# Optimization experiments

Measured on AMD Instinct MI355X. Metric: run time of the kernel, lower is better.

## Reference

```python
import jax, jax.numpy as jnp
import numpy as np

B, DZ, H, DY = 4096, 512, 2048, 10
N_STEPS = 64
SCALE = 0.02  # matches param_ulow/uhigh magnitude


def setup_inputs() -> dict:
    key = jax.random.key(0)
    ks = jax.random.split(key, 6)
    x = jax.random.normal(ks[0], (B, DZ), dtype=jnp.float32)
    A = jax.random.normal(ks[1], (DZ, DZ), dtype=jnp.float32) * SCALE
    W1 = jax.random.normal(ks[2], (H, DZ), dtype=jnp.float32) * SCALE
    b1 = jax.random.normal(ks[3], (H,), dtype=jnp.float32) * SCALE
    W2 = jax.random.normal(ks[4], (DY, H), dtype=jnp.float32) * SCALE
    b2 = jax.random.normal(ks[5], (DY,), dtype=jnp.float32) * SCALE
    return {"x": x, "A": A, "W1": W1, "b1": b1, "W2": W2, "b2": b2,
            "n_steps": N_STEPS}


def reference(x, A, W1, b1, W2, b2, n_steps):
    # Z0 = P @ x with P = I  => Z0 = x
    # dz/dt = einsum('ji,bi->bj', A, z) = z @ A.T ; explicit Euler on [0, 1]
    dt = jnp.float32(1.0 / n_steps)

    def euler_step(z, _):
        return z + dt * (z @ A.T), None

    zT, _ = jax.lax.scan(euler_step, x, None, length=n_steps)  # [B, DZ]
    # Q MLP (n_layers=3): Linear -> ReLU -> Linear
    h = jax.nn.relu(zT @ W1.T + b1)  # [B, H]
    y = h @ W2.T + b2                # [B, DY]
    return y
```

## Files before the change

### kernel.cpp

```cpp
#include <hip/hip_runtime.h>
#include <hip/hip_bf16.h>

#define B_SZ 4096
#define DZ   512
#define H_SZ 2048
#define DY   10

#define C2 0.4921875f
#define C3 0.158935546875f
#define C4 0.037872314453125f
#define C5 ((float)(7624512.0/1073741824.0))
#define C6 ((float)(74974368.0/68719476736.0))

typedef __attribute__((ext_vector_type(8))) __bf16 bf16x8;
typedef __attribute__((ext_vector_type(4))) float  f32x4;
typedef __attribute__((ext_vector_type(8))) unsigned short us8;

__device__ inline unsigned short f2bf(float f) {
    unsigned u = __float_as_uint(f);
    u += 0x7fffu + ((u >> 16) & 1u);
    return (unsigned short)(u >> 16);
}
__device__ inline float bf2f(unsigned short s) {
    return __uint_as_float(((unsigned)s) << 16);
}

__device__ __forceinline__ void gl16(const void* g, void* l) {
    __builtin_amdgcn_global_load_lds(
        (const __attribute__((address_space(1))) unsigned int*)(size_t)g,
        (__attribute__((address_space(3))) unsigned int*)(unsigned)(size_t)l,
        16, 0, 0);
}

union SqSmem {
    struct { unsigned short A[64 * 64]; unsigned short B[64 * 64]; } s;
    float epi[64 * 68];
};

__device__ __forceinline__ void stage64(const unsigned short* __restrict__ src,
                                        unsigned short* lds, int row_base,
                                        int kt, int t) {
    const int w = t >> 6, lane = t & 63;
#pragma unroll
    for (int i = 0; i < 2; ++i) {
        int o = w * 128 + i * 64 + lane;
        int row = o >> 3, cc = (o & 7) ^ (row & 7);
        gl16(&src[(size_t)(row_base + row) * 512 + kt * 64 + cc * 8],
             &lds[(size_t)(w * 128 + i * 64) * 8]);
    }
}

#define MFMA_STEP(acc)                                                        \
    {                                                                         \
        _Pragma("unroll")                                                     \
        for (int ks = 0; ks < 2; ++ks) {                                      \
            bf16x8 af[2], bfr[2];                                             \
            _Pragma("unroll")                                                 \
            for (int i = 0; i < 2; ++i) {                                     \
                int ra = wm + i * 16 + l16, ca = (ks * 4 + quad) ^ (ra & 7);  \
                af[i] = *(const bf16x8*)&sm.s.A[ra * 64 + ca * 8];            \
                int rb = wn + i * 16 + l16, cb = (ks * 4 + quad) ^ (rb & 7);  \
                bfr[i] = *(const bf16x8*)&sm.s.B[rb * 64 + cb * 8];           \
            }                                                                 \
            _Pragma("unroll")                                                 \
            for (int i = 0; i < 2; ++i)                                       \
                _Pragma("unroll")                                             \
                for (int j = 0; j < 2; ++j)                                   \
                    acc[i][j] = __builtin_amdgcn_mfma_f32_16x16x32_bf16(      \
                        af[i], bfr[j], acc[i][j], 0, 0, 0);                   \
        }                                                                     \
    }

#define ACC_TO_EPI(acc)                                                       \
    {                                                                         \
        _Pragma("unroll")                                                     \
        for (int i = 0; i < 2; ++i)                                           \
            _Pragma("unroll")                                                 \
            for (int j = 0; j < 2; ++j)                                       \
                _Pragma("unroll")                                             \
                for (int rr = 0; rr < 4; ++rr)                                \
                    sm.epi[(wm + i * 16 + quad * 4 + rr) * 68 +               \
                           wn + j * 16 + l16] = acc[i][j][rr];                \
        __syncthreads();                                                      \
    }

__device__ inline void gemm64_mfma(const unsigned short* __restrict__ Arows,
                                   const unsigned short* __restrict__ Brows,
                                   int m0, int n0, int t, SqSmem& sm) {
    const int lane = t & 63, w = t >> 6, quad = lane >> 4, l16 = lane & 15;
    const int wm = (w & 1) * 32, wn = (w >> 1) * 32;
    f32x4 acc[2][2];
#pragma unroll
    for (int i = 0; i < 2; ++i)
#pragma unroll
        for (int j = 0; j < 2; ++j) acc[i][j] = (f32x4){0.f, 0.f, 0.f, 0.f};
    for (int kt = 0; kt < 8; ++kt) {
        stage64(Arows, sm.s.A, m0, kt, t);
        stage64(Brows, sm.s.B, n0, kt, t);
        __syncthreads();
        MFMA_STEP(acc)
        __syncthreads();
    }
    ACC_TO_EPI(acc)
}

__device__ inline void gemm64_f32src(const float* __restrict__ Arows,
                                     const float* __restrict__ Bsrc,
                                     int m0, int n0, int t, SqSmem& sm) {
    const int lane = t & 63, w = t >> 6, quad = lane >> 4, l16 = lane & 15;
    const int wm = (w & 1) * 32, wn = (w >> 1) * 32;
    const int r = t >> 2, cq = t & 3;
    f32x4 acc[2][2];
#pragma unroll
    for (int i = 0; i < 2; ++i)
#pragma unroll
        for (int j = 0; j < 2; ++j) acc[i][j] = (f32x4){0.f, 0.f, 0.f, 0.f};
    for (int kt = 0; kt < 8; ++kt) {
        float va[16];
#pragma unroll
        for (int u = 0; u < 4; ++u) {
            float4 f = *(const float4*)&Arows[(size_t)(m0 + r) * 512 + kt * 64 + cq * 16 + u * 4];
            va[u * 4 + 0] = f.x; va[u * 4 + 1] = f.y;
            va[u * 4 + 2] = f.z; va[u * 4 + 3] = f.w;
        }
#pragma unroll
        for (int j2 = 0; j2 < 2; ++j2) {
            us8 h;
#pragma unroll
            for (int j = 0; j < 8; ++j) h[j] = f2bf(va[j2 * 8 + j]);
            int cc = cq * 2 + j2;
            *(us8*)&sm.s.A[r * 64 + (cc ^ (r & 7)) * 8] = h;
        }
#pragma unroll
        for (int u = 0; u < 4; ++u) {
            float4 f = *(const float4*)&Bsrc[(size_t)(kt * 64 + r) * 512 + n0 + cq * 16 + u * 4];
            float vv[4] = {f.x, f.y, f.z, f.w};
#pragma unroll
            for (int j = 0; j < 4; ++j) {
                int n = cq * 16 + u * 4 + j;
                sm.s.B[n * 64 + ((r >> 3) ^ (n & 7)) * 8 + (r & 7)] = f2bf(vv[j]);
            }
        }
        __syncthreads();
        MFMA_STEP(acc)
        __syncthreads();
    }
    ACC_TO_EPI(acc)
}

__device__ inline void epi_out_bf(unsigned short* __restrict__ dst, int m0,
                                  int n0, int t, SqSmem& sm) {
    const int r = t >> 2, cq = t & 3;
    us8 h0, h1;
#pragma unroll
    for (int j = 0; j < 8; ++j) {
        h0[j] = f2bf(sm.epi[r * 68 + cq * 16 + j]);
        h1[j] = f2bf(sm.epi[r * 68 + cq * 16 + 8 + j]);
    }
    *(us8*)&dst[(size_t)(m0 + r) * 512 + n0 + cq * 16]     = h0;
    *(us8*)&dst[(size_t)(m0 + r) * 512 + n0 + cq * 16 + 8] = h1;
}
__device__ inline void epi_out_bfT(unsigned short* __restrict__ dst, int m0,
                                   int n0, int t, SqSmem& sm) {
    const int cf = t >> 2, rq = t & 3;
    us8 o0, o1;
#pragma unroll
    for (int i = 0; i < 8; ++i) {
        o0[i] = f2bf(sm.epi[(rq * 16 + i) * 68 + cf]);
        o1[i] = f2bf(sm.epi[(rq * 16 + 8 + i) * 68 + cf]);
    }
    *(us8*)&dst[(size_t)(n0 + cf) * 512 + m0 + rq * 16]     = o0;
    *(us8*)&dst[(size_t)(n0 + cf) * 512 + m0 + rq * 16 + 8] = o1;
}

__global__ __launch_bounds__(256) void k_s1(
    const float* __restrict__ A, const float* __restrict__ x,
    const float* __restrict__ W1, const float* __restrict__ b2,
    unsigned short* __restrict__ A2_bf, unsigned short* __restrict__ A2T_bf,
    unsigned short* __restrict__ AT_bf, unsigned short* __restrict__ A_bf,
    unsigned short* __restrict__ x_bf, unsigned short* __restrict__ W1_bf,
    float* __restrict__ y) {
    __shared__ SqSmem sm;
    const int b = blockIdx.x, t = threadIdx.x;

    if (b < 64) {
        const int m0 = (b >> 3) * 64, n0 = (b & 7) * 64;
        gemm64_f32src(A, A, m0, n0, t, sm);
        epi_out_bf(A2_bf, m0, n0, t, sm);
        epi_out_bfT(A2T_bf, m0, n0, t, sm);
    } else if (b < 128) {
        const int bb = b - 64, m0 = (bb >> 3) * 64, n0 = (bb & 7) * 64;
        const int r = t >> 2, cq = t & 3;
#pragma unroll
        for (int u = 0; u < 4; ++u) {
            float4 f = *(const float4*)&A[(size_t)(m0 + r) * 512 + n0 + cq * 16 + u * 4];
            sm.epi[r * 68 + cq * 16 + u * 4 + 0] = f.x;
            sm.epi[r * 68 + cq * 16 + u * 4 + 1] = f.y;
            sm.epi[r * 68 + cq * 16 + u * 4 + 2] = f.z;
            sm.epi[r * 68 + cq * 16 + u * 4 + 3] = f.w;
        }
        __syncthreads();
        epi_out_bfT(AT_bf, m0, n0, t, sm);
    } else {
        const int gid = (b - 128) * 256 + t;
        const float4* x4 = (const float4*)x;
#pragma unroll
        for (int i = 0; i < 8; ++i) {
            int id = gid + i * 32768;
            float4 v0 = x4[(size_t)id * 2], v1 = x4[(size_t)id * 2 + 1];
            us8 o;
            o[0] = f2bf(v0.x); o[1] = f2bf(v0.y); o[2] = f2bf(v0.z); o[3] = f2bf(v0.w);
            o[4] = f2bf(v1.x); o[5] = f2bf(v1.y); o[6] = f2bf(v1.z); o[7] = f2bf(v1.w);
            *(us8*)&x_bf[(size_t)id * 8] = o;
        }
        const float4* w4 = (const float4*)W1;
#pragma unroll
        for (int i = 0; i < 4; ++i) {
            int id = gid + i * 32768;
            float4 v0 = w4[(size_t)id * 2], v1 = w4[(size_t)id * 2 + 1];
            us8 o;
            o[0] = f2bf(v0.x); o[1] = f2bf(v0.y); o[2] = f2bf(v0.z); o[3] = f2bf(v0.w);
            o[4] = f2bf(v1.x); o[5] = f2bf(v1.y); o[6] = f2bf(v1.z); o[7] = f2bf(v1.w);
            *(us8*)&W1_bf[(size_t)id * 8] = o;
        }
        {
            const float4* a4 = (const float4*)A;
            float4 v0 = a4[(size_t)gid * 2], v1 = a4[(size_t)gid * 2 + 1];
            us8 o;
            o[0] = f2bf(v0.x); o[1] = f2bf(v0.y); o[2] = f2bf(v0.z); o[3] = f2bf(v0.w);
            o[4] = f2bf(v1.x); o[5] = f2bf(v1.y); o[6] = f2bf(v1.z); o[7] = f2bf(v1.w);
            *(us8*)&A_bf[(size_t)gid * 8] = o;
        }
#pragma unroll
        for (int i = 0; i < 2; ++i) {
            int id = gid + i * 32768;
            if (id < B_SZ * DY) y[id] = b2[id % 10];
        }
    }
}

__global__ __launch_bounds__(256) void k_s2(
    const unsigned short* __restrict__ A2_bf,
    const unsigned short* __restrict__ A2T_bf,
    unsigned short* __restrict__ A4T_bf) {
    __shared__ SqSmem sm;
    const int b = blockIdx.x, t = threadIdx.x;
    const int m0 = (b >> 3) * 64, n0 = (b & 7) * 64;
    gemm64_mfma(A2_bf, A2T_bf, m0, n0, t, sm);
    epi_out_bfT(A4T_bf, m0, n0, t, sm);
}

__global__ __launch_bounds__(256) void k_s3(
    const unsigned short* __restrict__ A_bf,
    const unsigned short* __restrict__ A2_bf,
    const unsigned short* __restrict__ A2T_bf,
    const unsigned short* __restrict__ A4T_bf,
    const unsigned short* __restrict__ AT_bf,
    unsigned short* __restrict__ QpT_bf) {
    __shared__ SqSmem sm;
    const int b = blockIdx.x, t = threadIdx.x;
    const int m0 = (b >> 3) * 64, n0 = (b & 7) * 64;
    const int lane = t & 63, w = t >> 6, quad = lane >> 4, l16 = lane & 15;
    const int wm = (w & 1) * 32, wn = (w >> 1) * 32;
    f32x4 acc[2][2];
#pragma unroll
    for (int i = 0; i < 2; ++i)
#pragma unroll
        for (int j = 0; j < 2; ++j) acc[i][j] = (f32x4){0.f, 0.f, 0.f, 0.f};

#pragma unroll
    for (int pass = 0; pass < 2; ++pass) {
        const unsigned short* __restrict__ Bt = pass ? A4T_bf : A2T_bf;
        const float cA  = pass ? C5 : C3;
        const float cA2 = pass ? C6 : C4;
        for (int kt = 0; kt < 8; ++kt) {
            stage64(Bt, sm.s.B, n0, kt, t);
#pragma unroll
            for (int c = 0; c < 2; ++c) {
                int idx = c * 256 + t, row = idx >> 3, cc = idx & 7;
                int ccs = cc ^ (row & 7);
                size_t ga = (size_t)(m0 + row) * 512 + kt * 64 + cc * 8;
                us8 a  = *(const us8*)&A_bf[ga];
                us8 a2 = *(const us8*)&A2_bf[ga];
                us8 g;
#pragma unroll
                for (int j = 0; j < 8; ++j)
                    g[j] = f2bf(cA * bf2f(a[j]) + cA2 * bf2f(a2[j]));
                *(us8*)&sm.s.A[row * 64 + ccs * 8] = g;
            }
            __syncthreads();
            MFMA_STEP(acc)
            __syncthreads();
        }
    }
    ACC_TO_EPI(acc)

    const int cf = t >> 2, rq = t & 3;
    size_t gb = (size_t)(n0 + cf) * 512 + m0 + rq * 16;
    us8 at0  = *(const us8*)&AT_bf[gb],  at1  = *(const us8*)&AT_bf[gb + 8];
    us8 a2t0 = *(const us8*)&A2T_bf[gb], a2t1 = *(const us8*)&A2T_bf[gb + 8];
    us8 o0, o1;
#pragma unroll
    for (int i = 0; i < 8; ++i) {
        o0[i] = f2bf(bf2f(at0[i]) + C2 * bf2f(a2t0[i]) +
                     sm.epi[(rq * 16 + i) * 68 + cf]);
        o1[i] = f2bf(bf2f(at1[i]) + C2 * bf2f(a2t1[i]) +
                     sm.epi[(rq * 16 + 8 + i) * 68 + cf]);
    }
    *(us8*)&QpT_bf[gb]     = o0;
    *(us8*)&QpT_bf[gb + 8] = o1;
}

__global__ __launch_bounds__(256) void k_s4(
    const unsigned short* __restrict__ W1_bf,
    const unsigned short* __restrict__ QpT_bf,
    const float* __restrict__ W1, unsigned short* __restrict__ w1f) {
    __shared__ SqSmem sm;
    const int b = blockIdx.x, t = threadIdx.x;
    const int m0 = (b >> 3) * 64, n0 = (b & 7) * 64;
    gemm64_mfma(W1_bf, QpT_bf, m0, n0, t, sm);

    const int r = t >> 2, cq = t & 3;
    size_t gb = (size_t)(m0 + r) * 512 + n0 + cq * 16;
    float4 wa = *(const float4*)&W1[gb],      wbv = *(const float4*)&W1[gb + 4];
    float4 wc = *(const float4*)&W1[gb + 8],  wd  = *(const float4*)&W1[gb + 12];
    float wf[16] = {wa.x, wa.y, wa.z, wa.w, wbv.x, wbv.y, wbv.z, wbv.w,
                    wc.x, wc.y, wc.z, wc.w, wd.x,  wd.y,  wd.z,  wd.w};
    us8 h0, h1;
#pragma unroll
    for (int j = 0; j < 8; ++j) {
        h0[j] = f2bf(wf[j]     + sm.epi[r * 68 + cq * 16 + j]);
        h1[j] = f2bf(wf[8 + j] + sm.epi[r * 68 + cq * 16 + 8 + j]);
    }
    *(us8*)&w1f[gb]     = h0;
    *(us8*)&w1f[gb + 8] = h1;
}

union SmemU {
    struct { unsigned short A[128 * 64]; unsigned short B[128 * 64]; } s;
    struct { unsigned short h[128 * 136]; } e;
};

__global__ __launch_bounds__(256) void mlp_kernel(
    const unsigned short* __restrict__ x_bf,
    const unsigned short* __restrict__ w1f,
    const float* __restrict__ b1, const float* __restrict__ W2,
    float* __restrict__ y) {
    __shared__ SmemU sm;
    const int t    = threadIdx.x;
    const int lane = t & 63, w = t >> 6;
    const int quad = lane >> 4, l16 = lane & 15;
    const int wm = (w & 1) * 64, wn = (w >> 1) * 64;
    const int m0g = blockIdx.x * 128, n0g = blockIdx.y * 128;

    f32x4 acc[4][4];
#pragma unroll
    for (int i = 0; i < 4; ++i)
#pragma unroll
        for (int j = 0; j < 4; ++j) acc[i][j] = (f32x4){0.f, 0.f, 0.f, 0.f};

    for (int kt = 0; kt < 8; ++kt) {
#pragma unroll
        for (int i = 0; i < 4; ++i) {
            int o = w * 256 + i * 64 + lane;
            int row = o >> 3, cc = (o & 7) ^ (row & 7);
            gl16(&x_bf[(size_t)(m0g + row) * 512 + kt * 64 + cc * 8],
                 &sm.s.A[(size_t)(w * 256 + i * 64) * 8]);
        }
#pragma unroll
        for (int i = 0; i < 4; ++i) {
            int o = w * 256 + i * 64 + lane;
            int row = o >> 3, cc = (o & 7) ^ (row & 7);
            gl16(&w1f[(size_t)(n0g + row) * 512 + kt * 64 + cc * 8],
                 &sm.s.B[(size_t)(w * 256 + i * 64) * 8]);
        }
        __syncthreads();
#pragma unroll
        for (int ks = 0; ks < 2; ++ks) {
            bf16x8 af[4], bfr[4];
#pragma unroll
            for (int i = 0; i < 4; ++i) {
                int ra = wm + i * 16 + l16, ca = (ks * 4 + quad) ^ (ra & 7);
                af[i] = *(const bf16x8*)&sm.s.A[ra * 64 + ca * 8];
                int rb = wn + i * 16 + l16, cb = (ks * 4 + quad) ^ (rb & 7);
                bfr[i] = *(const bf16x8*)&sm.s.B[rb * 64 + cb * 8];
            }
#pragma unroll
            for (int i = 0; i < 4; ++i)
#pragma unroll
                for (int j = 0; j < 4; ++j)
                    acc[i][j] = __builtin_amdgcn_mfma_f32_16x16x32_bf16(
                        af[i], bfr[j], acc[i][j], 0, 0, 0);
        }
        __syncthreads();
    }

    float bias[4];
#pragma unroll
    for (int j = 0; j < 4; ++j) bias[j] = b1[n0g + wn + j * 16 + l16];
#pragma unroll
    for (int i = 0; i < 4; ++i)
#pragma unroll
        for (int j = 0; j < 4; ++j)
#pragma unroll
            for (int r = 0; r < 4; ++r) {
                float h = acc[i][j][r] + bias[j];
                h = h > 0.f ? h : 0.f;
                sm.e.h[(wm + i * 16 + quad * 4 + r) * 136 + wn + j * 16 + l16] =
                    f2bf(h);
            }
    __syncthreads();

    {
        bf16x8 wfrag[4];
#pragma unroll
        for (int kc = 0; kc < 4; ++kc) {
            us8 wb;
            if (l16 < DY) {
                const float* wp = &W2[(size_t)l16 * H_SZ + n0g + kc * 32 + quad * 8];
#pragma unroll
                for (int j = 0; j < 8; ++j) wb[j] = f2bf(wp[j]);
            } else {
#pragma unroll
                for (int j = 0; j < 8; ++j) wb[j] = 0;
            }
            wfrag[kc] = *(bf16x8*)&wb;
        }
#pragma unroll
        for (int hh = 0; hh < 2; ++hh) {
            const int mrow = w * 32 + hh * 16;
            f32x4 ay = (f32x4){0.f, 0.f, 0.f, 0.f};
#pragma unroll
            for (int kc = 0; kc < 4; ++kc) {
                bf16x8 af = *(const bf16x8*)&sm.e.h[(mrow + l16) * 136 +
                                                    kc * 32 + quad * 8];
                ay = __builtin_amdgcn_mfma_f32_16x16x32_bf16(af, wfrag[kc], ay,
                                                             0, 0, 0);
            }
            if (l16 < DY) {
#pragma unroll
                for (int r = 0; r < 4; ++r)
                    atomicAdd(&y[(size_t)(m0g + mrow + quad * 4 + r) * DY + l16],
                              ay[r]);
            }
        }
    }
}

extern "C" void kernel_launch(void* const* d_in, const int* in_sizes, int n_in,
                              void* d_out, int out_size, void* d_ws, size_t ws_size,
                              hipStream_t stream) {
    const float* x  = (const float*)d_in[0];
    const float* A  = (const float*)d_in[1];
    const float* W1 = (const float*)d_in[2];
    const float* b1 = (const float*)d_in[3];
    const float* W2 = (const float*)d_in[4];
    const float* b2 = (const float*)d_in[5];
    float* y = (float*)d_out;

    char* ws = (char*)d_ws;
    const size_t HMB = 512u * 1024, MB = 1u << 20;
    unsigned short* AT_bf  = (unsigned short*)(ws);
    unsigned short* A2_bf  = (unsigned short*)(ws + 1 * HMB);
    unsigned short* A2T_bf = (unsigned short*)(ws + 2 * HMB);
    unsigned short* A4T_bf = (unsigned short*)(ws + 3 * HMB);
    unsigned short* A_bf   = (unsigned short*)(ws + 4 * HMB);
    unsigned short* QpT_bf = (unsigned short*)(ws + 5 * HMB);
    unsigned short* w1f    = (unsigned short*)(ws + 3 * MB);
    unsigned short* W1_bf  = (unsigned short*)(ws + 5 * MB);
    unsigned short* x_bf   = (unsigned short*)(ws + 7 * MB);

    k_s1<<<256, 256, 0, stream>>>(A, x, W1, b2, A2_bf, A2T_bf, AT_bf, A_bf,
                                  x_bf, W1_bf, y);
    k_s2<<<64, 256, 0, stream>>>(A2_bf, A2T_bf, A4T_bf);
    k_s3<<<64, 256, 0, stream>>>(A_bf, A2_bf, A2T_bf, A4T_bf, AT_bf, QpT_bf);
    k_s4<<<256, 256, 0, stream>>>(W1_bf, QpT_bf, W1, w1f);
    mlp_kernel<<<dim3(32, 16), dim3(256), 0, stream>>>(x_bf, w1f, b1, W2, y);
}
```

Before: 142.1 us.

## Merge prep kernels into one persistent kernel with grid barriers

Fuses the four preparation kernels into one 256-block kernel that uses atomic-counter grid barriers between phases, so there are fewer kernel launches and launch gaps. It also restructures the polynomial computation: A4 and the first-pass combined term are now computed in parallel in one phase instead of serially. The added memset and the spin barriers cost something, and the design relies on all 256 blocks being co-resident; if they are not, the barriers deadlock.

Result: slower. 326.3 us (+129.7%).

```diff
diff --git a/kernel.cpp b/kernel.cpp
--- a/kernel.cpp
+++ b/kernel.cpp
@@ -30,6 +30,21 @@
         (const __attribute__((address_space(1))) unsigned int*)(size_t)g,
         (__attribute__((address_space(3))) unsigned int*)(unsigned)(size_t)l,
         16, 0, 0);
+}
+
+__device__ __forceinline__ void gridbar(unsigned* __restrict__ cnt,
+                                        unsigned target) {
+    __threadfence();
+    __syncthreads();
+    if (threadIdx.x == 0) {
+        __hip_atomic_fetch_add(cnt, 1u, __ATOMIC_ACQ_REL,
+                               __HIP_MEMORY_SCOPE_AGENT);
+        while (__hip_atomic_load(cnt, __ATOMIC_ACQUIRE,
+                                 __HIP_MEMORY_SCOPE_AGENT) < target)
+            __builtin_amdgcn_s_sleep(8);
+    }
+    __syncthreads();
+    __threadfence();
 }
 
 union SqSmem {
@@ -104,6 +119,40 @@
     ACC_TO_EPI(acc)
 }
 
+__device__ inline void gemm64_combineB(const unsigned short* __restrict__ Arows,
+                                       const unsigned short* __restrict__ X,
+                                       const unsigned short* __restrict__ Y,
+                                       float cx, float cy, int m0, int n0,
+                                       int t, SqSmem& sm) {
+    const int lane = t & 63, w = t >> 6, quad = lane >> 4, l16 = lane & 15;
+    const int wm = (w & 1) * 32, wn = (w >> 1) * 32;
+    f32x4 acc[2][2];
+#pragma unroll
+    for (int i = 0; i < 2; ++i)
+#pragma unroll
+        for (int j = 0; j < 2; ++j) acc[i][j] = (f32x4){0.f, 0.f, 0.f, 0.f};
+    for (int kt = 0; kt < 8; ++kt) {
+        stage64(Arows, sm.s.A, m0, kt, t);
+#pragma unroll
+        for (int c = 0; c < 2; ++c) {
+            int idx = c * 256 + t, row = idx >> 3, cc = idx & 7;
+            int ccs = cc ^ (row & 7);
+            size_t ga = (size_t)(n0 + row) * 512 + kt * 64 + cc * 8;
+            us8 xv = *(const us8*)&X[ga];
+            us8 yv = *(const us8*)&Y[ga];
+            us8 g;
+#pragma unroll
+            for (int j = 0; j < 8; ++j)
+                g[j] = f2bf(cx * bf2f(xv[j]) + cy * bf2f(yv[j]));
+            *(us8*)&sm.s.B[row * 64 + ccs * 8] = g;
+        }
+        __syncthreads();
+        MFMA_STEP(acc)
+        __syncthreads();
+    }
+    ACC_TO_EPI(acc)
+}
+
 __device__ inline void gemm64_f32src(const float* __restrict__ Arows,
                                      const float* __restrict__ Bsrc,
                                      int m0, int n0, int t, SqSmem& sm) {
@@ -173,13 +222,15 @@
     *(us8*)&dst[(size_t)(n0 + cf) * 512 + m0 + rq * 16 + 8] = o1;
 }
 
-__global__ __launch_bounds__(256) void k_s1(
+__global__ __launch_bounds__(256) void prep(
     const float* __restrict__ A, const float* __restrict__ x,
     const float* __restrict__ W1, const float* __restrict__ b2,
     unsigned short* __restrict__ A2_bf, unsigned short* __restrict__ A2T_bf,
     unsigned short* __restrict__ AT_bf, unsigned short* __restrict__ A_bf,
-    unsigned short* __restrict__ x_bf, unsigned short* __restrict__ W1_bf,
-    float* __restrict__ y) {
+    unsigned short* __restrict__ A4T_bf, unsigned short* __restrict__ GT_bf,
+    unsigned short* __restrict__ QpT_bf, unsigned short* __restrict__ x_bf,
+    unsigned short* __restrict__ W1_bf, unsigned short* __restrict__ w1f,
+    float* __restrict__ y, unsigned* __restrict__ cnt) {
     __shared__ SqSmem sm;
     const int b = blockIdx.x, t = threadIdx.x;
 
@@ -237,103 +288,58 @@
             if (id < B_SZ * DY) y[id] = b2[id % 10];
         }
     }
-}
-
-__global__ __launch_bounds__(256) void k_s2(
-    const unsigned short* __restrict__ A2_bf,
-    const unsigned short* __restrict__ A2T_bf,
-    unsigned short* __restrict__ A4T_bf) {
-    __shared__ SqSmem sm;
-    const int b = blockIdx.x, t = threadIdx.x;
-    const int m0 = (b >> 3) * 64, n0 = (b & 7) * 64;
-    gemm64_mfma(A2_bf, A2T_bf, m0, n0, t, sm);
-    epi_out_bfT(A4T_bf, m0, n0, t, sm);
-}
-
-__global__ __launch_bounds__(256) void k_s3(
-    const unsigned short* __restrict__ A_bf,
-    const unsigned short* __restrict__ A2_bf,
-    const unsigned short* __restrict__ A2T_bf,
-    const unsigned short* __restrict__ A4T_bf,
-    const unsigned short* __restrict__ AT_bf,
-    unsigned short* __restrict__ QpT_bf) {
-    __shared__ SqSmem sm;
-    const int b = blockIdx.x, t = threadIdx.x;
-    const int m0 = (b >> 3) * 64, n0 = (b & 7) * 64;
-    const int lane = t & 63, w = t >> 6, quad = lane >> 4, l16 = lane & 15;
-    const int wm = (w & 1) * 32, wn = (w >> 1) * 32;
-    f32x4 acc[2][2];
-#pragma unroll
-    for (int i = 0; i < 2; ++i)
-#pragma unroll
-        for (int j = 0; j < 2; ++j) acc[i][j] = (f32x4){0.f, 0.f, 0.f, 0.f};
-
-#pragma unroll
-    for (int pass = 0; pass < 2; ++pass) {
-        const unsigned short* __restrict__ Bt = pass ? A4T_bf : A2T_bf;
-        const float cA  = pass ? C5 : C3;
-        const float cA2 = pass ? C6 : C4;
-        for (int kt = 0; kt < 8; ++kt) {
-            stage64(Bt, sm.s.B, n0, kt, t);
-#pragma unroll
-            for (int c = 0; c < 2; ++c) {
-                int idx = c * 256 + t, row = idx >> 3, cc = idx & 7;
-                int ccs = cc ^ (row & 7);
-                size_t ga = (size_t)(m0 + row) * 512 + kt * 64 + cc * 8;
-                us8 a  = *(const us8*)&A_bf[ga];
-                us8 a2 = *(const us8*)&A2_bf[ga];
-                us8 g;
-#pragma unroll
-                for (int j = 0; j < 8; ++j)
-                    g[j] = f2bf(cA * bf2f(a[j]) + cA2 * bf2f(a2[j]));
-                *(us8*)&sm.s.A[row * 64 + ccs * 8] = g;
-            }
-            __syncthreads();
-            MFMA_STEP(acc)
-            __syncthreads();
-        }
-    }
-    ACC_TO_EPI(acc)
-
-    const int cf = t >> 2, rq = t & 3;
-    size_t gb = (size_t)(n0 + cf) * 512 + m0 + rq * 16;
-    us8 at0  = *(const us8*)&AT_bf[gb],  at1  = *(const us8*)&AT_bf[gb + 8];
-    us8 a2t0 = *(const us8*)&A2T_bf[gb], a2t1 = *(const us8*)&A2T_bf[gb + 8];
-    us8 o0, o1;
-#pragma unroll
-    for (int i = 0; i < 8; ++i) {
-        o0[i] = f2bf(bf2f(at0[i]) + C2 * bf2f(a2t0[i]) +
-                     sm.epi[(rq * 16 + i) * 68 + cf]);
-        o1[i] = f2bf(bf2f(at1[i]) + C2 * bf2f(a2t1[i]) +
-                     sm.epi[(rq * 16 + 8 + i) * 68 + cf]);
-    }
-    *(us8*)&QpT_bf[gb]     = o0;
-    *(us8*)&QpT_bf[gb + 8] = o1;
-}
-
-__global__ __launch_bounds__(256) void k_s4(
-    const unsigned short* __restrict__ W1_bf,
-    const unsigned short* __restrict__ QpT_bf,
-    const float* __restrict__ W1, unsigned short* __restrict__ w1f) {
-    __shared__ SqSmem sm;
-    const int b = blockIdx.x, t = threadIdx.x;
-    const int m0 = (b >> 3) * 64, n0 = (b & 7) * 64;
-    gemm64_mfma(W1_bf, QpT_bf, m0, n0, t, sm);
-
-    const int r = t >> 2, cq = t & 3;
-    size_t gb = (size_t)(m0 + r) * 512 + n0 + cq * 16;
-    float4 wa = *(const float4*)&W1[gb],      wbv = *(const float4*)&W1[gb + 4];
-    float4 wc = *(const float4*)&W1[gb + 8],  wd  = *(const float4*)&W1[gb + 12];
-    float wf[16] = {wa.x, wa.y, wa.z, wa.w, wbv.x, wbv.y, wbv.z, wbv.w,
-                    wc.x, wc.y, wc.z, wc.w, wd.x,  wd.y,  wd.z,  wd.w};
-    us8 h0, h1;
-#pragma unroll
-    for (int j = 0; j < 8; ++j) {
-        h0[j] = f2bf(wf[j]     + sm.epi[r * 68 + cq * 16 + j]);
-        h1[j] = f2bf(wf[8 + j] + sm.epi[r * 68 + cq * 16 + 8 + j]);
-    }
-    *(us8*)&w1f[gb]     = h0;
-    *(us8*)&w1f[gb + 8] = h1;
+    gridbar(cnt, 256);
+
+    if (b < 64) {
+        const int m0 = (b >> 3) * 64, n0 = (b & 7) * 64;
+        gemm64_combineB(A2T_bf, A_bf, A2_bf, C3, C4, m0, n0, t, sm);
+        epi_out_bf(GT_bf, m0, n0, t, sm);
+    } else if (b < 128) {
+        const int bb = b - 64, m0 = (bb >> 3) * 64, n0 = (bb & 7) * 64;
+        gemm64_mfma(A2T_bf, A2_bf, m0, n0, t, sm);
+        epi_out_bf(A4T_bf, m0, n0, t, sm);
+    }
+    gridbar(cnt, 512);
+
+    if (b < 64) {
+        const int m0 = (b >> 3) * 64, n0 = (b & 7) * 64;
+        gemm64_combineB(A4T_bf, A_bf, A2_bf, C5, C6, m0, n0, t, sm);
+        const int r = t >> 2, cq = t & 3;
+        size_t gb = (size_t)(m0 + r) * 512 + n0 + cq * 16;
+        us8 at0  = *(const us8*)&AT_bf[gb],  at1  = *(const us8*)&AT_bf[gb + 8];
+        us8 a2t0 = *(const us8*)&A2T_bf[gb], a2t1 = *(const us8*)&A2T_bf[gb + 8];
+        us8 gt0  = *(const us8*)&GT_bf[gb],  gt1  = *(const us8*)&GT_bf[gb + 8];
+        us8 o0, o1;
+#pragma unroll
+        for (int j = 0; j < 8; ++j) {
+            o0[j] = f2bf(bf2f(at0[j]) + C2 * bf2f(a2t0[j]) + bf2f(gt0[j]) +
+                         sm.epi[r * 68 + cq * 16 + j]);
+            o1[j] = f2bf(bf2f(at1[j]) + C2 * bf2f(a2t1[j]) + bf2f(gt1[j]) +
+                         sm.epi[r * 68 + cq * 16 + 8 + j]);
+        }
+        *(us8*)&QpT_bf[gb]     = o0;
+        *(us8*)&QpT_bf[gb + 8] = o1;
+    }
+    gridbar(cnt, 768);
+
+    {
+        const int m0 = (b >> 3) * 64, n0 = (b & 7) * 64;
+        gemm64_mfma(W1_bf, QpT_bf, m0, n0, t, sm);
+        const int r = t >> 2, cq = t & 3;
+        size_t gb = (size_t)(m0 + r) * 512 + n0 + cq * 16;
+        float4 wa = *(const float4*)&W1[gb],     wbv = *(const float4*)&W1[gb + 4];
+        float4 wc = *(const float4*)&W1[gb + 8], wd  = *(const float4*)&W1[gb + 12];
+        float wf[16] = {wa.x, wa.y, wa.z, wa.w, wbv.x, wbv.y, wbv.z, wbv.w,
+                        wc.x, wc.y, wc.z, wc.w, wd.x,  wd.y,  wd.z,  wd.w};
+        us8 h0, h1;
+#pragma unroll
+        for (int j = 0; j < 8; ++j) {
+            h0[j] = f2bf(wf[j]     + sm.epi[r * 68 + cq * 16 + j]);
+            h1[j] = f2bf(wf[8 + j] + sm.epi[r * 68 + cq * 16 + 8 + j]);
+        }
+        *(us8*)&w1f[gb]     = h0;
+        *(us8*)&w1f[gb + 8] = h1;
+    }
 }
 
 union SmemU {
@@ -465,15 +471,16 @@
     unsigned short* A2T_bf = (unsigned short*)(ws + 2 * HMB);
     unsigned short* A4T_bf = (unsigned short*)(ws + 3 * HMB);
     unsigned short* A_bf   = (unsigned short*)(ws + 4 * HMB);
-    unsigned short* QpT_bf = (unsigned short*)(ws + 5 * HMB);
-    unsigned short* w1f    = (unsigned short*)(ws + 3 * MB);
-    unsigned short* W1_bf  = (unsigned short*)(ws + 5 * MB);
-    unsigned short* x_bf   = (unsigned short*)(ws + 7 * MB);
-
-    k_s1<<<256, 256, 0, stream>>>(A, x, W1, b2, A2_bf, A2T_bf, AT_bf, A_bf,
-                                  x_bf, W1_bf, y);
-    k_s2<<<64, 256, 0, stream>>>(A2_bf, A2T_bf, A4T_bf);
-    k_s3<<<64, 256, 0, stream>>>(A_bf, A2_bf, A2T_bf, A4T_bf, AT_bf, QpT_bf);
-    k_s4<<<256, 256, 0, stream>>>(W1_bf, QpT_bf, W1, w1f);
+    unsigned short* GT_bf  = (unsigned short*)(ws + 5 * HMB);
+    unsigned short* QpT_bf = (unsigned short*)(ws + 6 * HMB);
+    unsigned short* w1f    = (unsigned short*)(ws + 4 * MB);
+    unsigned short* W1_bf  = (unsigned short*)(ws + 6 * MB);
+    unsigned short* x_bf   = (unsigned short*)(ws + 8 * MB);
+    unsigned*       cnt    = (unsigned*)(ws + 12 * MB);
+
+    hipMemsetAsync(cnt, 0, 128, stream);
+    prep<<<256, 256, 0, stream>>>(A, x, W1, b2, A2_bf, A2T_bf, AT_bf, A_bf,
+                                  A4T_bf, GT_bf, QpT_bf, x_bf, W1_bf, w1f, y,
+                                  cnt);
     mlp_kernel<<<dim3(32, 16), dim3(256), 0, stream>>>(x_bf, w1f, b1, W2, y);
 }
```
